# Optimization experiments

Measured on AMD Instinct MI355X. Metric: run time of the kernel, lower is better.

## Reference

```python
import jax, jax.numpy as jnp
import numpy as np

# static config matching init_kwargs / input_specs
SPATIAL = [(64, 64), (32, 32), (16, 16), (8, 8)]  # (H_l, W_l) per level
LEN = sum(h * w for h, w in SPATIAL)  # 5440
B, C, H, L, P = 4, 256, 8, 4, 4
DH = C // H
DFF = 1024
EPS = 1e-5


def layer_norm(x, g, b):
    m = x.mean(-1, keepdims=True)
    v = ((x - m) ** 2).mean(-1, keepdims=True)
    return (x - m) / jnp.sqrt(v + EPS) * g + b


def msda_core(value, sampling_locations, attn_weights):
    """Multi-scale deformable attention core (bilinear sample + weighted sum).
    value: [B, Len, H, DH]; sampling_locations: [B, Lq, H, L, P, 2] in [0,1];
    attn_weights: [B, Lq, H, L, P]. Returns [B, Lq, C].
    Matches grid_sample(bilinear, align_corners=False, padding_mode='zeros')."""
    Bn, Lq = sampling_locations.shape[0], sampling_locations.shape[1]
    out = jnp.zeros((Bn, H, Lq, DH), value.dtype)
    start = 0
    for l, (Hl, Wl) in enumerate(SPATIAL):
        vl = value[:, start:start + Hl * Wl]          # [B, Hl*Wl, H, DH]
        start += Hl * Wl
        vl = vl.transpose(0, 2, 1, 3)                  # [B, H, Hl*Wl, DH]
        loc = sampling_locations[:, :, :, l].transpose(0, 2, 1, 3, 4)  # [B,H,Lq,P,2]
        # align_corners=False: pixel = loc * size - 0.5
        px = loc[..., 0] * Wl - 0.5
        py = loc[..., 1] * Hl - 0.5
        x0 = jnp.floor(px); y0 = jnp.floor(py)
        wx1 = px - x0; wy1 = py - y0
        x0i = x0.astype(jnp.int32); y0i = y0.astype(jnp.int32)
        samp = jnp.zeros((Bn, H, Lq, P, DH), value.dtype)
        for dx, dy in ((0, 0), (1, 0), (0, 1), (1, 1)):
            ix = x0i + dx; iy = y0i + dy
            w = (wx1 if dx else 1.0 - wx1) * (wy1 if dy else 1.0 - wy1)
            valid = (ix >= 0) & (ix < Wl) & (iy >= 0) & (iy < Hl)
            idx = jnp.clip(iy, 0, Hl - 1) * Wl + jnp.clip(ix, 0, Wl - 1)  # [B,H,Lq,P]
            g = jnp.take_along_axis(vl, idx.reshape(Bn, H, -1)[..., None], axis=2)
            g = g.reshape(Bn, H, Lq, P, DH)
            samp = samp + g * (w * valid)[..., None]
        aw = attn_weights[:, :, :, l].transpose(0, 2, 1, 3)  # [B,H,Lq,P]
        out = out + (samp * aw[..., None]).sum(3)
    return out.transpose(0, 2, 1, 3).reshape(Bn, Lq, C)


def setup_inputs() -> dict:
    key = jax.random.key(0)
    ks = jax.random.split(key, 20)
    inp = {
        'src': jax.random.normal(ks[0], (B, LEN, C), jnp.float32),
        'pos': jax.random.normal(ks[1], (B, LEN, C), jnp.float32),
        'reference_points': jax.random.uniform(ks[2], (B, LEN, L, 2), jnp.float32),
        'spatial_shapes': jnp.array(SPATIAL, dtype=jnp.int32),
        'level_start_index': jnp.array(np.cumsum([0] + [h * w for h, w in SPATIAL[:-1]]), dtype=jnp.int32),
        'valid_ratios': jnp.ones((B, L, 2), jnp.float32),
        # MSDeformAttn params
        'w_off': jax.random.normal(ks[3], (C, H * L * P * 2), jnp.float32) * 0.01,
        'b_off': jax.random.normal(ks[4], (H * L * P * 2,), jnp.float32) * 0.5,
        'w_attn': jax.random.normal(ks[5], (C, H * L * P), jnp.float32) * 0.05,
        'b_attn': jnp.zeros((H * L * P,), jnp.float32),
        'w_val': jax.random.normal(ks[6], (C, C), jnp.float32) * 0.05,
        'b_val': jnp.zeros((C,), jnp.float32),
        'w_out': jax.random.normal(ks[7], (C, C), jnp.float32) * 0.05,
        'b_out': jnp.zeros((C,), jnp.float32),
        # norm1 + FFN + norm2 params
        'g1': jnp.ones((C,), jnp.float32), 'be1': jnp.zeros((C,), jnp.float32),
        'w1': jax.random.normal(ks[8], (C, DFF), jnp.float32) * 0.05,
        'b1': jnp.zeros((DFF,), jnp.float32),
        'w2': jax.random.normal(ks[9], (DFF, C), jnp.float32) * 0.05,
        'b2': jnp.zeros((C,), jnp.float32),
        'g2': jnp.ones((C,), jnp.float32), 'be2': jnp.zeros((C,), jnp.float32),
    }
    return inp


def reference(src, pos, reference_points, spatial_shapes, level_start_index, valid_ratios,
              w_off, b_off, w_attn, b_attn, w_val, b_val, w_out, b_out,
              g1, be1, w1, b1, w2, b2, g2, be2):
    Bn, Lq, _ = src.shape
    q = src + pos  # with_pos_embed
    off = (q @ w_off + b_off).reshape(Bn, Lq, H, L, P, 2)
    aw = jax.nn.softmax((q @ w_attn + b_attn).reshape(Bn, Lq, H, L * P), axis=-1)
    aw = aw.reshape(Bn, Lq, H, L, P)
    # offset normalizer is (W_l, H_l) per level
    norm = jnp.array([[w, h] for h, w in SPATIAL], dtype=src.dtype)  # [L, 2]
    loc = reference_points[:, :, None, :, None, :] + off / norm[None, None, None, :, None, :]
    value = (src @ w_val + b_val).reshape(Bn, Lq, H, DH)  # padding_mask is None
    attn_out = msda_core(value, loc, aw) @ w_out + b_out
    x = layer_norm(src + attn_out, g1, be1)
    ffn = jax.nn.relu(x @ w1 + b1) @ w2 + b2
    return layer_norm(x + ffn, g2, be2)
```

## Files before the change

kernel.cpp:

```cpp
#include <hip/hip_runtime.h>
#include <hip/hip_fp16.h>
#include <math.h>

#define LEN   5440
#define NTOK  21760
#define DFF   1024
#define LEPS  1e-5f

typedef __attribute__((ext_vector_type(8))) _Float16 f16x8;
typedef __attribute__((ext_vector_type(4))) float f32x4;

__device__ __forceinline__ float4 f4_add(float4 a, float4 b) {
    return make_float4(a.x + b.x, a.y + b.y, a.z + b.z, a.w + b.w);
}

__device__ __forceinline__ __half2 u2h2(unsigned u) {
    union { unsigned u; __half2 h; } c; c.u = u; return c.h;
}

__device__ __forceinline__ void gload_lds16(const void* g, void* l) {
    __builtin_amdgcn_global_load_lds(
        (const __attribute__((address_space(1))) unsigned int*)g,
        (__attribute__((address_space(3))) unsigned int*)l, 16, 0, 0);
}

__device__ __forceinline__ int swz8(int lin, int nwg) {
    const int q = nwg >> 3, r = nwg & 7;
    const int x = lin & 7, j = lin >> 3;
    return (x < r ? x * (q + 1) : r * (q + 1) + (x - r) * q) + j;
}

__global__ __launch_bounds__(256) void pack_k(const float* __restrict__ w_off,
                                              const float* __restrict__ w_attn,
                                              const float* __restrict__ w_val,
                                              const float* __restrict__ b_off,
                                              const float* __restrict__ b_attn,
                                              const float* __restrict__ b_val,
                                              const float* __restrict__ w_out,
                                              const float* __restrict__ w1,
                                              const float* __restrict__ w2,
                                              __half* __restrict__ WcatT,
                                              __half* __restrict__ woutT,
                                              __half* __restrict__ w1T,
                                              __half* __restrict__ w2T,
                                              float* __restrict__ bcat) {
    const int i = blockIdx.x * 256 + threadIdx.x;
    if (i < 163840) {
        const int c = i >> 8, k = i & 255;
        float v;
        if (c < 256)      v = w_off[k * 256 + c];
        else if (c < 384) v = w_attn[k * 128 + (c - 256)];
        else              v = w_val[k * 256 + (c - 384)];
        WcatT[i] = __float2half(v);
    } else if (i < 229376) {
        const int j = i - 163840, c = j >> 8, k = j & 255;
        woutT[j] = __float2half(w_out[k * 256 + c]);
    } else if (i < 491520) {
        const int j = i - 229376, c = j >> 8, k = j & 255;
        w1T[j] = __float2half(w1[k * 1024 + c]);
    } else if (i < 753664) {
        const int j = i - 491520, c = j >> 10, k = j & 1023;
        w2T[j] = __float2half(w2[k * 256 + c]);
    }
    if (i < 640) {
        bcat[i] = (i < 256) ? b_off[i] : (i < 384) ? b_attn[i - 256] : b_val[i - 384];
    }
}

__global__ __launch_bounds__(256) void cvt_k(const float* __restrict__ src,
                                             const float* __restrict__ pos,
                                             __half* __restrict__ qh,
                                             __half* __restrict__ srch) {
    const size_t i = (size_t)blockIdx.x * 256 + threadIdx.x;
    float4 s = *(const float4*)&src[i * 4];
    float4 p = *(const float4*)&pos[i * 4];
    union { __half2 h[2]; uint2 u; } Q, S;
    Q.h[0] = __floats2half2_rn(s.x + p.x, s.y + p.y);
    Q.h[1] = __floats2half2_rn(s.z + p.z, s.w + p.w);
    S.h[0] = __floats2half2_rn(s.x, s.y);
    S.h[1] = __floats2half2_rn(s.z, s.w);
    *(uint2*)&qh[i * 4]   = Q.u;
    *(uint2*)&srch[i * 4] = S.u;
}

template <int BM, int BN, int OMODE>
__global__ __launch_bounds__(256) void hgemm_k(const __half* __restrict__ Aq,
                                               const __half* __restrict__ Av,
                                               const __half* __restrict__ Bt,
                                               const float* __restrict__ bias,
                                               float* __restrict__ Cf,
                                               __half* __restrict__ Ch,
                                               int NnF, int NnH, int K, int colSwitch) {
    constexpr int KC = 256;
    constexpr int MR = BM / 32;
    constexpr int NR = BN / 32;
    __shared__ __half As[BM][KC];
    __shared__ __half Bs[BN][KC];

    const int nbx = gridDim.x;
    const int tile = swz8(blockIdx.y * nbx + blockIdx.x, nbx * gridDim.y);
    const int bx = tile % nbx, by = tile / nbx;

    const int tid = threadIdx.x;
    const int lane = tid & 63;
    const int wave = tid >> 6;
    const int wr = (wave >> 1) * (BM / 2);
    const int wc = (wave & 1) * (BN / 2);

    const __half* __restrict__ Ah = (bx * BN < colSwitch) ? Aq : Av;

    const int rl = lane >> 5, ck = lane & 31;
    const int xm = (2 * wave + rl) & 7;
    const int colx = ((ck ^ xm) << 3);
    const __half* Ap = Ah + (size_t)(by * BM + 2 * wave + rl) * K + colx;
    const __half* Bp = Bt + (size_t)(bx * BN + 2 * wave + rl) * K + colx;

    const int fr = lane & 15;
    const int hi = lane >> 4;
    const int xr = fr & 7;

    f32x4 acc[MR][NR];
#pragma unroll
    for (int m = 0; m < MR; ++m)
#pragma unroll
        for (int n = 0; n < NR; ++n) acc[m][n] = (f32x4){0.f, 0.f, 0.f, 0.f};

    for (int kc = 0; kc < K; kc += KC) {
        if (kc) __syncthreads();
#pragma unroll
        for (int j = 0; j < BM / 8; ++j)
            gload_lds16(Ap + ((size_t)(8 * j) * K + kc), &As[2 * wave + 8 * j][0]);
#pragma unroll
        for (int j = 0; j < BN / 8; ++j)
            gload_lds16(Bp + ((size_t)(8 * j) * K + kc), &Bs[2 * wave + 8 * j][0]);
        __syncthreads();

        const char* Ab = (const char*)&As[0][0];
        const char* Bb = (const char*)&Bs[0][0];
#pragma unroll
        for (int kk = 0; kk < KC / 32; ++kk) {
            const int cb = (kk << 2) + hi;
            const int co = ((cb ^ xr) << 4);
            f16x8 af[MR], bf[NR];
#pragma unroll
            for (int m = 0; m < MR; ++m)
                af[m] = *(const f16x8*)(Ab + (wr + m * 16 + fr) * (KC * 2) + co);
#pragma unroll
            for (int n = 0; n < NR; ++n)
                bf[n] = *(const f16x8*)(Bb + (wc + n * 16 + fr) * (KC * 2) + co);
#pragma unroll
            for (int m = 0; m < MR; ++m)
#pragma unroll
                for (int n = 0; n < NR; ++n)
                    acc[m][n] = __builtin_amdgcn_mfma_f32_16x16x32_f16(af[m], bf[n], acc[m][n], 0, 0, 0);
        }
    }

    const int rowb = by * BM + wr + hi * 4;
    const int colb = bx * BN + wc + fr;
    float bn[NR];
#pragma unroll
    for (int n = 0; n < NR; ++n) bn[n] = bias[colb + n * 16];
    const bool vhalf = (OMODE == 2) || (OMODE == 3 && bx * BN >= colSwitch);
    const int colh = (OMODE == 3) ? (colb - colSwitch) : colb;
#pragma unroll
    for (int m = 0; m < MR; ++m) {
#pragma unroll
        for (int r = 0; r < 4; ++r) {
            const int row = rowb + m * 16 + r;
#pragma unroll
            for (int n = 0; n < NR; ++n) {
                float v = acc[m][n][r] + bn[n];
                if (OMODE == 2) v = fmaxf(v, 0.f);
                if (vhalf) Ch[(size_t)row * NnH + colh + n * 16] = __float2half(v);
                else       Cf[(size_t)row * NnF + colb + n * 16] = v;
            }
        }
    }
}

__global__ __launch_bounds__(256) void msda_kernel(const float* __restrict__ C1a,
                                                   const __half* __restrict__ Vh,
                                                   const float* __restrict__ refp,
                                                   __half* __restrict__ out) {
    __shared__ int      sOff[16][17][4];
    __shared__ unsigned sWh[16][17][4];
    const int tid = threadIdx.x;
    const int gi = tid >> 4;
    const int si = tid & 15;
    const int tile = swz8(blockIdx.x, gridDim.x);
    const int n = tile * 2 + (gi >> 3);
    const int h = gi & 7;
    const int b = n / LEN;

    {
        const int l = si >> 2, p = si & 3;
        const float lg = C1a[(size_t)n * 384 + 256 + h * 16 + si];
        float mx = lg;
#pragma unroll
        for (int m = 1; m < 16; m <<= 1) mx = fmaxf(mx, __shfl_xor(mx, m, 16));
        const float e = __expf(lg - mx);
        float sum = e;
#pragma unroll
        for (int m = 1; m < 16; m <<= 1) sum += __shfl_xor(sum, m, 16);
        const float aw = e / sum;

        const int Wi[4] = {64, 32, 16, 8};
        const int st[4] = {0, 4096, 5120, 5376};
        const int W = Wi[l];
        const float Wf = (float)W;
        const float rx = refp[((size_t)n * 4 + l) * 2 + 0];
        const float ry = refp[((size_t)n * 4 + l) * 2 + 1];
        const float2 oxy = *(const float2*)&C1a[(size_t)n * 384 + (((h * 4 + l) * 4 + p) * 2)];
        const float lx = rx + oxy.x / Wf;
        const float ly = ry + oxy.y / Wf;
        const float px = lx * Wf - 0.5f;
        const float py = ly * Wf - 0.5f;
        const float x0f = floorf(px), y0f = floorf(py);
        const float wx1 = px - x0f, wy1 = py - y0f;
        const int x0 = (int)x0f, y0 = (int)y0f;
#pragma unroll
        for (int c = 0; c < 4; ++c) {
            const int dx = c & 1, dy = c >> 1;
            const int ix = x0 + dx, iy = y0 + dy;
            const float wgt = (dx ? wx1 : 1.f - wx1) * (dy ? wy1 : 1.f - wy1);
            const bool valid = (ix >= 0) && (ix < W) && (iy >= 0) && (iy < W);
            const int ixc = min(max(ix, 0), W - 1);
            const int iyc = min(max(iy, 0), W - 1);
            const int pos = st[l] + iyc * W + ixc;
            sOff[gi][si][c] = ((b * LEN + pos) << 9) + (h << 6);
            const float wa = valid ? (aw * wgt) : 0.f;
            const unsigned wu = (unsigned)__half_as_ushort(__float2half_rn(wa));
            sWh[gi][si][c] = wu | (wu << 16);
        }
    }
    __syncthreads();

    const int cbyte = (si & 3) * 16;
    const int sb = (si >> 2) * 4;
    __half2 acc0 = u2h2(0), acc1 = u2h2(0), acc2 = u2h2(0), acc3 = u2h2(0);
    const char* Vb = (const char*)Vh;
#pragma unroll
    for (int t = 0; t < 4; ++t) {
        const int s = sb + t;
        const int4  off = *(const int4*)&sOff[gi][s][0];
        const uint4 wq  = *(const uint4*)&sWh[gi][s][0];
        union { uint4 u; __half2 h2[4]; } v0, v1, v2, v3;
        v0.u = *(const uint4*)(Vb + off.x + cbyte);
        v1.u = *(const uint4*)(Vb + off.y + cbyte);
        v2.u = *(const uint4*)(Vb + off.z + cbyte);
        v3.u = *(const uint4*)(Vb + off.w + cbyte);
        const __half2 w0 = u2h2(wq.x), w1 = u2h2(wq.y), w2 = u2h2(wq.z), w3 = u2h2(wq.w);
        acc0 = __hfma2(v0.h2[0], w0, acc0);
        acc1 = __hfma2(v0.h2[1], w0, acc1);
        acc2 = __hfma2(v0.h2[2], w0, acc2);
        acc3 = __hfma2(v0.h2[3], w0, acc3);
        acc0 = __hfma2(v1.h2[0], w1, acc0);
        acc1 = __hfma2(v1.h2[1], w1, acc1);
        acc2 = __hfma2(v1.h2[2], w1, acc2);
        acc3 = __hfma2(v1.h2[3], w1, acc3);
        acc0 = __hfma2(v2.h2[0], w2, acc0);
        acc1 = __hfma2(v2.h2[1], w2, acc1);
        acc2 = __hfma2(v2.h2[2], w2, acc2);
        acc3 = __hfma2(v2.h2[3], w2, acc3);
        acc0 = __hfma2(v3.h2[0], w3, acc0);
        acc1 = __hfma2(v3.h2[1], w3, acc1);
        acc2 = __hfma2(v3.h2[2], w3, acc2);
        acc3 = __hfma2(v3.h2[3], w3, acc3);
    }
    float f0 = __low2float(acc0), f1 = __high2float(acc0);
    float f2 = __low2float(acc1), f3 = __high2float(acc1);
    float f4 = __low2float(acc2), f5 = __high2float(acc2);
    float f6 = __low2float(acc3), f7 = __high2float(acc3);
#pragma unroll
    for (int m = 4; m <= 8; m <<= 1) {
        f0 += __shfl_xor(f0, m, 64);
        f1 += __shfl_xor(f1, m, 64);
        f2 += __shfl_xor(f2, m, 64);
        f3 += __shfl_xor(f3, m, 64);
        f4 += __shfl_xor(f4, m, 64);
        f5 += __shfl_xor(f5, m, 64);
        f6 += __shfl_xor(f6, m, 64);
        f7 += __shfl_xor(f7, m, 64);
    }
    if (si < 4) {
        union { __half2 h2[4]; uint4 u; } O;
        O.h2[0] = __floats2half2_rn(f0, f1);
        O.h2[1] = __floats2half2_rn(f2, f3);
        O.h2[2] = __floats2half2_rn(f4, f5);
        O.h2[3] = __floats2half2_rn(f6, f7);
        *(uint4*)&out[(size_t)n * 256 + h * 32 + si * 8] = O.u;
    }
}

template <bool WH>
__global__ __launch_bounds__(256) void ln_kernel(const float* __restrict__ Y,
                                                 const float* __restrict__ R,
                                                 const float* __restrict__ gm,
                                                 const float* __restrict__ bt,
                                                 float* __restrict__ O,
                                                 __half* __restrict__ OH) {
    const int wave = threadIdx.x >> 6, lane = threadIdx.x & 63;
    const int n = blockIdx.x * 4 + wave;
    const size_t base = (size_t)n * 256 + lane * 4;
    float4 y = *(const float4*)&Y[base];
    float4 r = *(const float4*)&R[base];
    float4 v = f4_add(y, r);
    float s = v.x + v.y + v.z + v.w;
#pragma unroll
    for (int m = 1; m < 64; m <<= 1) s += __shfl_xor(s, m, 64);
    const float mean = s * (1.f / 256.f);
    const float dx = v.x - mean, dy = v.y - mean, dz = v.z - mean, dw = v.w - mean;
    float ss = dx * dx + dy * dy + dz * dz + dw * dw;
#pragma unroll
    for (int m = 1; m < 64; m <<= 1) ss += __shfl_xor(ss, m, 64);
    const float rstd = rsqrtf(ss * (1.f / 256.f) + LEPS);
    const float4 g4 = *(const float4*)&gm[lane * 4];
    const float4 b4 = *(const float4*)&bt[lane * 4];
    float4 o;
    o.x = dx * rstd * g4.x + b4.x;
    o.y = dy * rstd * g4.y + b4.y;
    o.z = dz * rstd * g4.z + b4.z;
    o.w = dw * rstd * g4.w + b4.w;
    *(float4*)&O[base] = o;
    if (WH) {
        union { __half2 h[2]; uint2 u; } Hh;
        Hh.h[0] = __floats2half2_rn(o.x, o.y);
        Hh.h[1] = __floats2half2_rn(o.z, o.w);
        *(uint2*)&OH[base] = Hh.u;
    }
}

extern "C" void kernel_launch(void* const* d_in, const int* in_sizes, int n_in,
                              void* d_out, int out_size, void* d_ws, size_t ws_size,
                              hipStream_t stream) {
    const float* src   = (const float*)d_in[0];
    const float* pos   = (const float*)d_in[1];
    const float* refp  = (const float*)d_in[2];
    const float* w_off  = (const float*)d_in[6];
    const float* b_off  = (const float*)d_in[7];
    const float* w_attn = (const float*)d_in[8];
    const float* b_attn = (const float*)d_in[9];
    const float* w_val  = (const float*)d_in[10];
    const float* b_val  = (const float*)d_in[11];
    const float* w_out  = (const float*)d_in[12];
    const float* b_out  = (const float*)d_in[13];
    const float* g1     = (const float*)d_in[14];
    const float* be1    = (const float*)d_in[15];
    const float* w1     = (const float*)d_in[16];
    const float* b1     = (const float*)d_in[17];
    const float* w2     = (const float*)d_in[18];
    const float* b2     = (const float*)d_in[19];
    const float* g2     = (const float*)d_in[20];
    const float* be2    = (const float*)d_in[21];

    float* ws = (float*)d_ws;
    float*  C1a   = ws + 0;
    __half* Vh    = (__half*)(ws + 8355840);
    __half* msdah = (__half*)(ws + 11141120);
    float*  xbuf  = ws + 13926400;
    __half* xh    = (__half*)(ws + 19496960);
    __half* hh    = (__half*)(ws + 22282240);
    __half* qh    = (__half*)(ws + 33423360);
    __half* srch  = (__half*)(ws + 36208640);
    __half* WcatT = (__half*)(ws + 38993920);
    __half* woutT = (__half*)(ws + 39075840);
    __half* w1T   = (__half*)(ws + 39108608);
    __half* w2T   = (__half*)(ws + 39239680);
    float*  bcat  = ws + 39370752;
    float*  ybuf  = C1a;

    pack_k<<<2944, 256, 0, stream>>>(w_off, w_attn, w_val, b_off, b_attn, b_val,
                                     w_out, w1, w2, WcatT, woutT, w1T, w2T, bcat);
    cvt_k<<<5440, 256, 0, stream>>>(src, pos, qh, srch);

    hgemm_k<128, 128, 3><<<dim3(5, 170), 256, 0, stream>>>(
        qh, srch, WcatT, bcat, C1a, Vh, 384, 256, 256, 384);

    msda_kernel<<<NTOK / 2, 256, 0, stream>>>(C1a, Vh, refp, msdah);

    hgemm_k<64, 64, 0><<<dim3(4, 340), 256, 0, stream>>>(
        msdah, msdah, woutT, b_out, ybuf, nullptr, 256, 256, 256, 1 << 30);

    ln_kernel<true><<<NTOK / 4, 256, 0, stream>>>(ybuf, src, g1, be1, xbuf, xh);

    hgemm_k<128, 128, 2><<<dim3(8, 170), 256, 0, stream>>>(
        xh, xh, w1T, b1, nullptr, hh, 1024, 1024, 256, 1 << 30);

    hgemm_k<64, 64, 0><<<dim3(4, 340), 256, 0, stream>>>(
        hh, hh, w2T, b2, ybuf, nullptr, 256, 256, 1024, 1 << 30);

    ln_kernel<false><<<NTOK / 4, 256, 0, stream>>>(ybuf, xbuf, g2, be2, (float*)d_out, nullptr);
}
```

Baseline: 285.9 us.

## Fuse output and FFN2 GEMMs with residual add and LayerNorm

Adds a GEMM kernel whose blocks each own 64 full rows of 256 output columns, so the epilogue can add bias and residual and compute the row mean and variance with shuffles plus a small LDS exchange. This replaces two GEMM + LayerNorm kernel pairs and removes the fp32 intermediate write and read of ybuf along with two launches. The trade-offs are a grid of only 340 blocks with no double buffering, a single-pass variance (E[x^2]-mean^2) that is less numerically robust, and workspace buffers that are now aliased to shrink the footprint.

```diff
diff --git a/kernel.cpp b/kernel.cpp
--- a/kernel.cpp
+++ b/kernel.cpp
@@ -179,6 +179,149 @@
     }
 }
 
+template <int KTOT, bool LN1MODE>
+__global__ __launch_bounds__(256) void hgemm_ln_k(const __half* __restrict__ A,
+                                                  const __half* __restrict__ Bt,
+                                                  const float* __restrict__ bias,
+                                                  const float* __restrict__ RES,
+                                                  const float* __restrict__ gm,
+                                                  const float* __restrict__ be,
+                                                  float* __restrict__ Of,
+                                                  __half* __restrict__ Oh) {
+    constexpr int KC = 128;
+    __shared__ __half As[64][KC];
+    __shared__ __half Bs[256][KC];
+
+    const int by = swz8(blockIdx.x, gridDim.x);
+    const int tid = threadIdx.x;
+    const int lane = tid & 63;
+    const int wave = tid >> 6;
+    const int wr = (wave >> 1) * 32;
+    const int wc = (wave & 1) * 128;
+
+    const int lrw = lane >> 4;
+    const int u   = lane & 15;
+    const int x0 = u ^ lrw;
+    const int x1 = u ^ (4 + lrw);
+    const __half* pA0 = A + (size_t)(by * 64 + wave * 16 + lrw) * KTOT + (x0 << 3);
+    const __half* pA1 = A + (size_t)(by * 64 + wave * 16 + 4 + lrw) * KTOT + (x1 << 3);
+    const __half* pB0 = Bt + (size_t)(wave * 64 + lrw) * KTOT + (x0 << 3);
+    const __half* pB1 = Bt + (size_t)(wave * 64 + 4 + lrw) * KTOT + (x1 << 3);
+
+    const int fr = lane & 15;
+    const int hi = lane >> 4;
+    const int xr = fr & 7;
+
+    f32x4 acc[2][8];
+#pragma unroll
+    for (int m = 0; m < 2; ++m)
+#pragma unroll
+        for (int n = 0; n < 8; ++n) acc[m][n] = (f32x4){0.f, 0.f, 0.f, 0.f};
+
+    for (int kc = 0; kc < KTOT; kc += KC) {
+        if (kc) __syncthreads();
+        gload_lds16(pA0 + kc, &As[wave * 16 + 0][0]);
+        gload_lds16(pA1 + kc, &As[wave * 16 + 4][0]);
+        gload_lds16(pA0 + kc + (size_t)8 * KTOT, &As[wave * 16 + 8][0]);
+        gload_lds16(pA1 + kc + (size_t)8 * KTOT, &As[wave * 16 + 12][0]);
+#pragma unroll
+        for (int j = 0; j < 8; ++j) {
+            gload_lds16(pB0 + kc + (size_t)(8 * j) * KTOT, &Bs[wave * 64 + 8 * j + 0][0]);
+            gload_lds16(pB1 + kc + (size_t)(8 * j) * KTOT, &Bs[wave * 64 + 8 * j + 4][0]);
+        }
+        __syncthreads();
+
+        const char* Ab = (const char*)&As[0][0];
+        const char* Bb = (const char*)&Bs[0][0];
+#pragma unroll
+        for (int kk = 0; kk < 4; ++kk) {
+            const int co = (((kk << 2) + hi) ^ xr) << 4;
+            f16x8 af[2], bf[8];
+#pragma unroll
+            for (int m = 0; m < 2; ++m)
+                af[m] = *(const f16x8*)(Ab + (wr + m * 16 + fr) * (KC * 2) + co);
+#pragma unroll
+            for (int n = 0; n < 8; ++n)
+                bf[n] = *(const f16x8*)(Bb + (wc + n * 16 + fr) * (KC * 2) + co);
+#pragma unroll
+            for (int m = 0; m < 2; ++m)
+#pragma unroll
+                for (int n = 0; n < 8; ++n)
+                    acc[m][n] = __builtin_amdgcn_mfma_f32_16x16x32_f16(af[m], bf[n], acc[m][n], 0, 0, 0);
+        }
+    }
+
+    const int rowl = wr + hi * 4;
+    const int colb = wc + fr;
+    float bn[8], gw[8], bw[8];
+#pragma unroll
+    for (int n = 0; n < 8; ++n) {
+        bn[n] = bias[colb + n * 16];
+        gw[n] = gm[colb + n * 16];
+        bw[n] = be[colb + n * 16];
+    }
+
+    float s1[2][4], s2[2][4];
+#pragma unroll
+    for (int m = 0; m < 2; ++m) {
+#pragma unroll
+        for (int r = 0; r < 4; ++r) {
+            const float* resp = RES + (size_t)(by * 64 + rowl + m * 16 + r) * 256 + colb;
+            float a1 = 0.f, a2 = 0.f;
+#pragma unroll
+            for (int n = 0; n < 8; ++n) {
+                float v = acc[m][n][r] + bn[n] + resp[n * 16];
+                acc[m][n][r] = v;
+                a1 += v;
+                a2 = fmaf(v, v, a2);
+            }
+            s1[m][r] = a1;
+            s2[m][r] = a2;
+        }
+    }
+#pragma unroll
+    for (int d = 1; d < 16; d <<= 1) {
+#pragma unroll
+        for (int m = 0; m < 2; ++m)
+#pragma unroll
+            for (int r = 0; r < 4; ++r) {
+                s1[m][r] += __shfl_xor(s1[m][r], d, 16);
+                s2[m][r] += __shfl_xor(s2[m][r], d, 16);
+            }
+    }
+    float* sRed = (float*)&As[0][0];
+    __syncthreads();
+    if (fr == 0) {
+#pragma unroll
+        for (int m = 0; m < 2; ++m)
+#pragma unroll
+            for (int r = 0; r < 4; ++r) {
+                const int lr = rowl + m * 16 + r;
+                sRed[((wave & 1) * 64 + lr) * 2 + 0] = s1[m][r];
+                sRed[((wave & 1) * 64 + lr) * 2 + 1] = s2[m][r];
+            }
+    }
+    __syncthreads();
+#pragma unroll
+    for (int m = 0; m < 2; ++m) {
+#pragma unroll
+        for (int r = 0; r < 4; ++r) {
+            const int lr = rowl + m * 16 + r;
+            const float t1 = s1[m][r] + sRed[(((wave & 1) ^ 1) * 64 + lr) * 2 + 0];
+            const float t2 = s2[m][r] + sRed[(((wave & 1) ^ 1) * 64 + lr) * 2 + 1];
+            const float mean = t1 * (1.f / 256.f);
+            const float rstd = rsqrtf(t2 * (1.f / 256.f) - mean * mean + LEPS);
+            const size_t ro = (size_t)(by * 64 + lr) * 256 + colb;
+#pragma unroll
+            for (int n = 0; n < 8; ++n) {
+                const float o = (acc[m][n][r] - mean) * rstd * gw[n] + bw[n];
+                Of[ro + n * 16] = o;
+                if (LN1MODE) Oh[ro + n * 16] = __float2half(o);
+            }
+        }
+    }
+}
+
 __global__ __launch_bounds__(256) void msda_kernel(const float* __restrict__ C1a,
                                                    const __half* __restrict__ Vh,
                                                    const float* __restrict__ refp,
@@ -293,44 +436,6 @@
     }
 }
 
-template <bool WH>
-__global__ __launch_bounds__(256) void ln_kernel(const float* __restrict__ Y,
-                                                 const float* __restrict__ R,
-                                                 const float* __restrict__ gm,
-                                                 const float* __restrict__ bt,
-                                                 float* __restrict__ O,
-                                                 __half* __restrict__ OH) {
-    const int wave = threadIdx.x >> 6, lane = threadIdx.x & 63;
-    const int n = blockIdx.x * 4 + wave;
-    const size_t base = (size_t)n * 256 + lane * 4;
-    float4 y = *(const float4*)&Y[base];
-    float4 r = *(const float4*)&R[base];
-    float4 v = f4_add(y, r);
-    float s = v.x + v.y + v.z + v.w;
-#pragma unroll
-    for (int m = 1; m < 64; m <<= 1) s += __shfl_xor(s, m, 64);
-    const float mean = s * (1.f / 256.f);
-    const float dx = v.x - mean, dy = v.y - mean, dz = v.z - mean, dw = v.w - mean;
-    float ss = dx * dx + dy * dy + dz * dz + dw * dw;
-#pragma unroll
-    for (int m = 1; m < 64; m <<= 1) ss += __shfl_xor(ss, m, 64);
-    const float rstd = rsqrtf(ss * (1.f / 256.f) + LEPS);
-    const float4 g4 = *(const float4*)&gm[lane * 4];
-    const float4 b4 = *(const float4*)&bt[lane * 4];
-    float4 o;
-    o.x = dx * rstd * g4.x + b4.x;
-    o.y = dy * rstd * g4.y + b4.y;
-    o.z = dz * rstd * g4.z + b4.z;
-    o.w = dw * rstd * g4.w + b4.w;
-    *(float4*)&O[base] = o;
-    if (WH) {
-        union { __half2 h[2]; uint2 u; } Hh;
-        Hh.h[0] = __floats2half2_rn(o.x, o.y);
-        Hh.h[1] = __floats2half2_rn(o.z, o.w);
-        *(uint2*)&OH[base] = Hh.u;
-    }
-}
-
 extern "C" void kernel_launch(void* const* d_in, const int* in_sizes, int n_in,
                               void* d_out, int out_size, void* d_ws, size_t ws_size,
                               hipStream_t stream) {
@@ -361,14 +466,13 @@
     float*  xbuf  = ws + 13926400;
     __half* xh    = (__half*)(ws + 19496960);
     __half* hh    = (__half*)(ws + 22282240);
-    __half* qh    = (__half*)(ws + 33423360);
-    __half* srch  = (__half*)(ws + 36208640);
-    __half* WcatT = (__half*)(ws + 38993920);
-    __half* woutT = (__half*)(ws + 39075840);
-    __half* w1T   = (__half*)(ws + 39108608);
-    __half* w2T   = (__half*)(ws + 39239680);
-    float*  bcat  = ws + 39370752;
-    float*  ybuf  = C1a;
+    __half* qh    = (__half*)(ws + 22282240);
+    __half* srch  = (__half*)(ws + 13926400);
+    __half* WcatT = (__half*)(ws + 33423360);
+    __half* woutT = (__half*)(ws + 33505280);
+    __half* w1T   = (__half*)(ws + 33538048);
+    __half* w2T   = (__half*)(ws + 33669120);
+    float*  bcat  = ws + 33800192;
 
     pack_k<<<2944, 256, 0, stream>>>(w_off, w_attn, w_val, b_off, b_attn, b_val,
                                      w_out, w1, w2, WcatT, woutT, w1T, w2T, bcat);
@@ -379,16 +483,12 @@
 
     msda_kernel<<<NTOK / 2, 256, 0, stream>>>(C1a, Vh, refp, msdah);
 
-    hgemm_k<64, 64, 0><<<dim3(4, 340), 256, 0, stream>>>(
-        msdah, msdah, woutT, b_out, ybuf, nullptr, 256, 256, 256, 1 << 30);
-
-    ln_kernel<true><<<NTOK / 4, 256, 0, stream>>>(ybuf, src, g1, be1, xbuf, xh);
+    hgemm_ln_k<256, true><<<340, 256, 0, stream>>>(
+        msdah, woutT, b_out, src, g1, be1, xbuf, xh);
 
     hgemm_k<128, 128, 2><<<dim3(8, 170), 256, 0, stream>>>(
         xh, xh, w1T, b1, nullptr, hh, 1024, 1024, 256, 1 << 30);
 
-    hgemm_k<64, 64, 0><<<dim3(4, 340), 256, 0, stream>>>(
-        hh, hh, w2T, b2, ybuf, nullptr, 256, 256, 1024, 1 << 30);
-
-    ln_kernel<false><<<NTOK / 4, 256, 0, stream>>>(ybuf, xbuf, g2, be2, (float*)d_out, nullptr);
-}
+    hgemm_ln_k<1024, false><<<340, 256, 0, stream>>>(
+        hh, w2T, b2, xbuf, g2, be2, (float*)d_out, nullptr);
+}
```

Result: faster. 266.7 us (-6.7%).
